# Performance work log

Measured on AMD Instinct MI355X. Metric: run time of the kernel, lower is better.

The kernel has to match this reference:

```python
import jax, jax.numpy as jnp
import numpy as np

HEADS = 16
D_MODEL = 1024
HEAD_DIM = D_MODEL // HEADS


def setup_inputs() -> dict:
    key = jax.random.key(0)
    ks = jax.random.split(key, 11)
    B, S = 4, 2048
    scale_in = 1.0 / np.sqrt(HEAD_DIM)
    scale_out = 1.0 / np.sqrt(D_MODEL)
    return {
        "values": jax.random.normal(ks[0], (B, S, D_MODEL), dtype=jnp.float32),
        "keys": jax.random.normal(ks[1], (B, S, D_MODEL), dtype=jnp.float32),
        "query": jax.random.normal(ks[2], (B, S, D_MODEL), dtype=jnp.float32),
        "wq": jax.random.normal(ks[3], (HEAD_DIM, HEAD_DIM), dtype=jnp.float32) * scale_in,
        "bq": jax.random.normal(ks[4], (HEAD_DIM,), dtype=jnp.float32) * 0.01,
        "wk": jax.random.normal(ks[5], (HEAD_DIM, HEAD_DIM), dtype=jnp.float32) * scale_in,
        "bk": jax.random.normal(ks[6], (HEAD_DIM,), dtype=jnp.float32) * 0.01,
        "wv": jax.random.normal(ks[7], (HEAD_DIM, HEAD_DIM), dtype=jnp.float32) * scale_in,
        "bv": jax.random.normal(ks[8], (HEAD_DIM,), dtype=jnp.float32) * 0.01,
        "wo": jax.random.normal(ks[9], (D_MODEL, D_MODEL), dtype=jnp.float32) * scale_out,
        "bo": jax.random.normal(ks[10], (D_MODEL,), dtype=jnp.float32) * 0.01,
    }


def reference(values, keys, query, wq, bq, wk, bk, wv, bv, wo, bo):
    B, Sq = query.shape[0], query.shape[1]
    Sk, Sv = keys.shape[1], values.shape[1]
    # reshape to (n, s, h, d); per-head linear shares one [d,d] weight across heads
    v = values.reshape(B, Sv, HEADS, HEAD_DIM) @ wv.T + bv
    k = keys.reshape(B, Sk, HEADS, HEAD_DIM) @ wk.T + bk
    q = query.reshape(B, Sq, HEADS, HEAD_DIM) @ wq.T + bq
    # scores scaled by sqrt(d_model) (as in original, NOT sqrt(head_dim))
    energy = jnp.einsum("nqhd,nkhd->nhqk", q, k)
    attn = jax.nn.softmax(energy / jnp.sqrt(jnp.float32(D_MODEL)), axis=-1)
    out = jnp.einsum("nhqk,nkhd->nqhd", attn, v).reshape(B, Sq, D_MODEL)
    return out @ wo.T + bo
```

## Files before the change

### kernel.cpp

```cpp
#include <hip/hip_runtime.h>

typedef unsigned short u16;
typedef short  bfrag  __attribute__((ext_vector_type(8), may_alias));
typedef unsigned long long ull_a __attribute__((may_alias));
typedef int    int_a  __attribute__((may_alias));
typedef int    i4_a   __attribute__((ext_vector_type(4), may_alias));
typedef float  f4_a   __attribute__((ext_vector_type(4), may_alias));
typedef unsigned u32x2 __attribute__((ext_vector_type(2)));
typedef __attribute__((ext_vector_type(4)))  float facc4;
typedef __attribute__((ext_vector_type(16))) float facc16;

#define SEQ   2048
#define NHEAD 16
#define HD    64
#define DM    1024
#define BH    64
#define NTOK  8192
#define QSC   0.04508422f

#if defined(__has_builtin)
#if __has_builtin(__builtin_amdgcn_cvt_pk_bf16_f32)
#define HAS_CVT_PK 1
#endif
#if __has_builtin(__builtin_amdgcn_permlane32_swap)
#define HAS_PLSWAP 1
#endif
#endif
#ifndef HAS_CVT_PK
#define HAS_CVT_PK 0
#endif
#ifndef HAS_PLSWAP
#define HAS_PLSWAP 0
#endif

__device__ __forceinline__ u16 f2bf(float f){
  union { float f; unsigned u; } x; x.f = f;
  unsigned r = x.u + 0x7FFFu + ((x.u >> 16) & 1u);
  return (u16)(r >> 16);
}
__device__ __forceinline__ unsigned pk2(float a, float b){
#if HAS_CVT_PK
  auto r = __builtin_amdgcn_cvt_pk_bf16_f32(a, b);
  union { decltype(r) v; unsigned u; } x; x.v = r; return x.u;
#else
  return (unsigned)f2bf(a) | ((unsigned)f2bf(b) << 16);
#endif
}
__device__ __forceinline__ unsigned long long pk4(float a, float b, float c, float d){
  return (unsigned long long)pk2(a,b) | ((unsigned long long)pk2(c,d) << 32);
}
__device__ __forceinline__ void swap32(unsigned &a, unsigned &b){
#if HAS_PLSWAP
  u32x2 r = __builtin_amdgcn_permlane32_swap(a, b, false, false);
  a = r[0]; b = r[1];
#else
  int lane = threadIdx.x & 63; int hh = lane >> 5;
  unsigned pa = (unsigned)__shfl_xor((int)a, 32, 64);
  unsigned pb = (unsigned)__shfl_xor((int)b, 32, 64);
  unsigned na = hh ? pb : a;
  unsigned nb = hh ? b  : pa;
  a = na; b = nb;
#endif
}
__device__ __forceinline__ bfrag ld8f(const float* p){
  f4_a a = *(const f4_a*)p;
  f4_a b = *(const f4_a*)(p + 4);
  union { bfrag v; unsigned u[4]; } r;
  r.u[0] = pk2(a[0],a[1]); r.u[1] = pk2(a[2],a[3]);
  r.u[2] = pk2(b[0],b[1]); r.u[3] = pk2(b[2],b[3]);
  return r.v;
}
__device__ __forceinline__ void stage16(const u16* g, u16* l){
  __builtin_amdgcn_global_load_lds((const __attribute__((address_space(1))) void*)g,
                                   (__attribute__((address_space(3))) void*)l, 16, 0, 0);
}

__global__ __launch_bounds__(256) void k_wconv(
  const float* __restrict__ wo, u16* __restrict__ dst)
{
  long i = ((long)blockIdx.x * 256 + threadIdx.x) * 8;
  f4_a a = *(const f4_a*)(wo + i);
  f4_a b = *(const f4_a*)(wo + i + 4);
  ull_a* p = (ull_a*)(dst + i);
  p[0] = pk4(a[0],a[1],a[2],a[3]);
  p[1] = pk4(b[0],b[1],b[2],b[3]);
}

__global__ __launch_bounds__(256, 4) void k_proj(
  const float* __restrict__ vin, const float* __restrict__ kin, const float* __restrict__ qin,
  const float* __restrict__ wq, const float* __restrict__ wk, const float* __restrict__ wv,
  const float* __restrict__ bq, const float* __restrict__ bk, const float* __restrict__ bv,
  u16* __restrict__ qo, u16* __restrict__ ko, u16* __restrict__ vt)
{
  __shared__ __align__(16) u16 LT[128*68];
  int tid = threadIdx.x;
  int wid = tid >> 6, lane = tid & 63;
  int ln = lane & 31, hh = lane >> 5;
  int h  = blockIdx.y;
  int t0 = blockIdx.x * 128;
  int b  = t0 >> 11;
  int s0 = t0 & 2047;
  int bh = b * NHEAD + h;
  int tok = t0 + wid*32 + ln;
  long xoff = (long)tok * DM + h * HD;

  auto run_mm = [&](const float* __restrict__ x, const float* __restrict__ w,
                    facc16* acc){
    bfrag bx[4], aw[2][4];
    #pragma unroll
    for (int ks = 0; ks < 4; ks++)
      bx[ks] = ld8f(x + xoff + ks*16 + hh*8);
    #pragma unroll
    for (int dt = 0; dt < 2; dt++)
      #pragma unroll
      for (int ks = 0; ks < 4; ks++)
        aw[dt][ks] = ld8f(w + (dt*32 + ln)*HD + ks*16 + hh*8);
    #pragma unroll
    for (int dt = 0; dt < 2; dt++){
      facc16 a;
      #pragma unroll
      for (int r = 0; r < 16; r++) a[r] = 0.f;
      #pragma unroll
      for (int ks = 0; ks < 4; ks++)
        a = __builtin_amdgcn_mfma_f32_32x32x16_bf16(aw[dt][ks], bx[ks], a, 0,0,0);
      acc[dt] = a;
    }
  };

  {
    facc16 acc[2]; run_mm(vin, wv, acc);
    int s = s0 + wid*32 + ln;
    long vb = (long)bh * HD * SEQ + s;
    #pragma unroll
    for (int dt = 0; dt < 2; dt++)
      #pragma unroll
      for (int g = 0; g < 4; g++){
        f4_a bb = *(const f4_a*)(bv + dt*32 + g*8 + 4*hh);
        #pragma unroll
        for (int j = 0; j < 4; j++){
          int d = dt*32 + g*8 + 4*hh + j;
          vt[vb + (long)d * SEQ] = f2bf(acc[dt][g*4+j] + bb[j]);
        }
      }
  }

  {
    facc16 acc[2]; run_mm(qin, wq, acc);
    int row = wid*32 + ln;
    #pragma unroll
    for (int dt = 0; dt < 2; dt++)
      #pragma unroll
      for (int g = 0; g < 4; g++){
        f4_a bb = *(const f4_a*)(bq + dt*32 + g*8 + 4*hh);
        *(ull_a*)&LT[row*68 + dt*32 + g*8 + 4*hh] =
          pk4((acc[dt][g*4+0]+bb[0])*QSC, (acc[dt][g*4+1]+bb[1])*QSC,
              (acc[dt][g*4+2]+bb[2])*QSC, (acc[dt][g*4+3]+bb[3])*QSC);
      }
  }
  __syncthreads();
  {
    int rr = tid >> 1, half = tid & 1;
    long gb = ((long)bh * SEQ + s0 + rr) * HD + half*32;
    #pragma unroll
    for (int j = 0; j < 4; j++)
      *(i4_a*)(qo + gb + j*8) = *(const i4_a*)&LT[rr*68 + half*32 + j*8];
  }
  __syncthreads();

  {
    facc16 acc[2]; run_mm(kin, wk, acc);
    int row = wid*32 + ln;
    #pragma unroll
    for (int dt = 0; dt < 2; dt++)
      #pragma unroll
      for (int g = 0; g < 4; g++){
        f4_a bb = *(const f4_a*)(bk + dt*32 + g*8 + 4*hh);
        *(ull_a*)&LT[row*68 + dt*32 + g*8 + 4*hh] =
          pk4(acc[dt][g*4+0]+bb[0], acc[dt][g*4+1]+bb[1],
              acc[dt][g*4+2]+bb[2], acc[dt][g*4+3]+bb[3]);
      }
  }
  __syncthreads();
  {
    int rr = tid >> 1, half = tid & 1;
    long gb = ((long)bh * SEQ + s0 + rr) * HD + half*32;
    #pragma unroll
    for (int j = 0; j < 4; j++)
      *(i4_a*)(ko + gb + j*8) = *(const i4_a*)&LT[rr*68 + half*32 + j*8];
  }
}

__global__ __launch_bounds__(512, 4) void k_attn(
  const u16* __restrict__ qws, const u16* __restrict__ kws, const u16* __restrict__ vt,
  u16* __restrict__ aout)
{
  __shared__ __align__(16) u16 KV[2][2][64*64];
  int tid = threadIdx.x;
  int wid = tid >> 6, lane = tid & 63;
  int ln = lane & 31, hh = lane >> 5;
  int bid = blockIdx.x;
  int xcd = bid & 7, lix = bid >> 3;
  int bh = xcd * 8 + (lix >> 3);
  int q0 = (lix & 7) * 256 + wid * 32;
  long base = (long)bh * SEQ * HD;

  int srow   = lane >> 3;
  int schunk = (lane & 7) ^ srow;

  bfrag qf[4];
  #pragma unroll
  for (int ks = 0; ks < 4; ks++)
    qf[ks] = *(const bfrag*)(qws + base + (long)(q0 + ln)*HD + ks*16 + hh*8);

  facc16 OO0, OO1;
  #pragma unroll
  for (int r = 0; r < 16; r++){ OO0[r] = 0.f; OO1[r] = 0.f; }
  float l_ = 0.f;

  stage16(kws + base + (long)(wid*8 + srow)*HD + schunk*8,  &KV[0][0][wid*512]);
  stage16(vt  + base + (long)(wid*8 + srow)*SEQ + schunk*8, &KV[0][1][wid*512]);

  auto tile = [&](int buf, int kt){
    __syncthreads();
    if (kt + 1 < 32){
      int k0n = (kt + 1) * 64;
      stage16(kws + base + (long)(k0n + wid*8 + srow)*HD + schunk*8, &KV[buf^1][0][wid*512]);
      stage16(vt  + base + (long)(wid*8 + srow)*SEQ + k0n + schunk*8, &KV[buf^1][1][wid*512]);
    }

    facc16 E0, E1;
    #pragma unroll
    for (int r = 0; r < 16; r++){ E0[r] = 0.f; E1[r] = 0.f; }
    __builtin_amdgcn_s_setprio(1);
    #pragma unroll
    for (int ks = 0; ks < 4; ks++){
      int sw = ((2*ks + hh) ^ (ln & 7)) * 8;
      bfrag kf0 = *(const bfrag*)&KV[buf][0][ ln      *64 + sw];
      bfrag kf1 = *(const bfrag*)&KV[buf][0][(32 + ln)*64 + sw];
      E0 = __builtin_amdgcn_mfma_f32_32x32x16_bf16(kf0, qf[ks], E0, 0,0,0);
      E1 = __builtin_amdgcn_mfma_f32_32x32x16_bf16(kf1, qf[ks], E1, 0,0,0);
    }
    __builtin_amdgcn_s_setprio(0);

    float rs = 0.f;
    #pragma unroll
    for (int r = 0; r < 16; r++){
      float p0 = __builtin_amdgcn_exp2f(E0[r]);
      float p1 = __builtin_amdgcn_exp2f(E1[r]);
      E0[r] = p0; E1[r] = p1; rs += p0 + p1;
    }
    l_ += rs;

    bfrag pf[4];
    #pragma unroll
    for (int half = 0; half < 2; half++){
      const facc16& P = half ? E1 : E0;
      #pragma unroll
      for (int k2 = 0; k2 < 2; k2++){
        int rb = k2 * 8;
        unsigned A0 = pk2(P[rb+0], P[rb+1]);
        unsigned A1 = pk2(P[rb+2], P[rb+3]);
        unsigned B0 = pk2(P[rb+4], P[rb+5]);
        unsigned B1 = pk2(P[rb+6], P[rb+7]);
        swap32(A0, B0);
        swap32(A1, B1);
        union { bfrag v; unsigned u[4]; } t;
        t.u[0] = A0; t.u[1] = A1; t.u[2] = B0; t.u[3] = B1;
        pf[half*2 + k2] = t.v;
      }
    }

    __builtin_amdgcn_s_setprio(1);
    #pragma unroll
    for (int ks = 0; ks < 4; ks++){
      int sw = ((2*ks + hh) ^ (ln & 7)) * 8;
      bfrag vf0 = *(const bfrag*)&KV[buf][1][ ln      *64 + sw];
      bfrag vf1 = *(const bfrag*)&KV[buf][1][(32 + ln)*64 + sw];
      OO0 = __builtin_amdgcn_mfma_f32_32x32x16_bf16(vf0, pf[ks], OO0, 0,0,0);
      OO1 = __builtin_amdgcn_mfma_f32_32x32x16_bf16(vf1, pf[ks], OO1, 0,0,0);
    }
    __builtin_amdgcn_s_setprio(0);
  };

  for (int kt = 0; kt < 32; kt += 2){
    tile(0, kt);
    tile(1, kt + 1);
  }

  l_ += __shfl_xor(l_, 32, 64);
  float inv = 1.0f / l_;
  int b_ = bh >> 4, h_ = bh & 15;
  long orow = ((long)(b_ * SEQ + q0 + ln) * NHEAD + h_) * HD;
  #pragma unroll
  for (int g = 0; g < 4; g++){
    *(ull_a*)(aout + orow +      8*g + 4*hh) =
      pk4(OO0[4*g]*inv, OO0[4*g+1]*inv, OO0[4*g+2]*inv, OO0[4*g+3]*inv);
    *(ull_a*)(aout + orow + 32 + 8*g + 4*hh) =
      pk4(OO1[4*g]*inv, OO1[4*g+1]*inv, OO1[4*g+2]*inv, OO1[4*g+3]*inv);
  }
}

__global__ __launch_bounds__(256) void k_oproj(
  const u16* __restrict__ A, const u16* __restrict__ Bw,
  const float* __restrict__ bo, float* __restrict__ out)
{
  __shared__ __align__(16) u16 As[128*64];
  __shared__ __align__(16) u16 Bs[128*64];
  int tid  = threadIdx.x;
  int wid  = tid >> 6, lane = tid & 63;
  int quad = lane >> 4, col = lane & 15;
  int m0 = blockIdx.x * 128;
  int n0 = blockIdx.y * 128;
  int wm = (wid & 1) * 64, wn = (wid >> 1) * 64;

  facc4 acc[4][4];
  #pragma unroll
  for (int i = 0; i < 4; i++)
    #pragma unroll
    for (int j = 0; j < 4; j++) acc[i][j] = {0.f,0.f,0.f,0.f};

  int srow = wid*8 + (lane >> 3);
  int scol = (lane & 7) * 8;
  const u16* Ag = A  + (long)(m0 + srow) * DM + scol;
  const u16* Bg = Bw + (long)(n0 + srow) * DM + scol;

  for (int k0 = 0; k0 < DM; k0 += 64){
    __syncthreads();
    #pragma unroll
    for (int j = 0; j < 4; j++){
      stage16(Ag + (long)j*32*DM + k0, &As[(j*32 + wid*8)*64]);
      stage16(Bg + (long)j*32*DM + k0, &Bs[(j*32 + wid*8)*64]);
    }
    __syncthreads();

    #pragma unroll
    for (int ks = 0; ks < 2; ks++){
      bfrag af[4], bf[4];
      #pragma unroll
      for (int i = 0; i < 4; i++)
        af[i] = *(const bfrag*)&As[(wm + i*16 + col)*64 + ks*32 + quad*8];
      #pragma unroll
      for (int i = 0; i < 4; i++)
        bf[i] = *(const bfrag*)&Bs[(wn + i*16 + col)*64 + ks*32 + quad*8];
      #pragma unroll
      for (int i = 0; i < 4; i++)
        #pragma unroll
        for (int j = 0; j < 4; j++)
          acc[i][j] = __builtin_amdgcn_mfma_f32_16x16x32_bf16(af[i], bf[j], acc[i][j], 0,0,0);
    }
  }

  #pragma unroll
  for (int j = 0; j < 4; j++){
    int n = n0 + wn + j*16 + col;
    float bias = bo[n];
    #pragma unroll
    for (int i = 0; i < 4; i++){
      long mrow = m0 + wm + i*16 + quad*4;
      #pragma unroll
      for (int r = 0; r < 4; r++)
        out[(mrow + r) * DM + n] = acc[i][j][r] + bias;
    }
  }
}

extern "C" void kernel_launch(void* const* d_in, const int* in_sizes, int n_in,
                              void* d_out, int out_size, void* d_ws, size_t ws_size,
                              hipStream_t stream)
{
  const float* values = (const float*)d_in[0];
  const float* keys   = (const float*)d_in[1];
  const float* query  = (const float*)d_in[2];
  const float* wq = (const float*)d_in[3];
  const float* bq = (const float*)d_in[4];
  const float* wk = (const float*)d_in[5];
  const float* bk = (const float*)d_in[6];
  const float* wv = (const float*)d_in[7];
  const float* bv = (const float*)d_in[8];
  const float* wo = (const float*)d_in[9];
  const float* bo = (const float*)d_in[10];

  const long N = 8388608;
  u16* qws  = (u16*)d_ws;
  u16* kws  = qws  + N;
  u16* vws  = kws  + N;
  u16* vtws = vws  + N;
  u16* wob  = vtws + N;
  u16* aws  = vws;

  k_wconv <<<512,           256, 0, stream>>>(wo, wob);
  k_proj  <<<dim3(64, 16),  256, 0, stream>>>(values, keys, query, wq, wk, wv,
                                              bq, bk, bv, qws, kws, vtws);
  k_attn  <<<512,           512, 0, stream>>>(qws, kws, vtws, aws);
  k_oproj <<<dim3(64, 8),   256, 0, stream>>>(aws, wob, bo, (float*)d_out);
}
```

Before: 288.3 us.

## Double-buffer LDS, swizzle shared layout, and XCD-aware tile mapping in output projection

Turns the output-projection GEMM's shared-memory staging into a two-buffer pipeline, so the next K-tile's global loads are issued before the current tile's MFMAs and one barrier per step is removed. It also XOR-swizzles the 16-byte chunks in LDS to reduce bank conflicts on fragment reads. Block indices are remapped so each XCD handles a contiguous band of M rows for better L2 reuse. The cost is twice the LDS per block, which may limit occupancy, offset only partly by the launch-bounds hint.

```diff
diff --git a/kernel.cpp b/kernel.cpp
--- a/kernel.cpp
+++ b/kernel.cpp
@@ -300,17 +300,19 @@
   }
 }
 
-__global__ __launch_bounds__(256) void k_oproj(
+__global__ __launch_bounds__(256, 2) void k_oproj(
   const u16* __restrict__ A, const u16* __restrict__ Bw,
   const float* __restrict__ bo, float* __restrict__ out)
 {
-  __shared__ __align__(16) u16 As[128*64];
-  __shared__ __align__(16) u16 Bs[128*64];
+  __shared__ __align__(16) u16 As[2][128*64];
+  __shared__ __align__(16) u16 Bs[2][128*64];
   int tid  = threadIdx.x;
   int wid  = tid >> 6, lane = tid & 63;
   int quad = lane >> 4, col = lane & 15;
-  int m0 = blockIdx.x * 128;
-  int n0 = blockIdx.y * 128;
+  int bid = blockIdx.x;
+  int xcd = bid & 7, lix = bid >> 3;
+  int m0 = (xcd * 8 + (lix >> 3)) * 128;
+  int n0 = (lix & 7) * 128;
   int wm = (wid & 1) * 64, wn = (wid >> 1) * 64;
 
   facc4 acc[4][4];
@@ -319,35 +321,51 @@
     #pragma unroll
     for (int j = 0; j < 4; j++) acc[i][j] = {0.f,0.f,0.f,0.f};
 
-  int srow = wid*8 + (lane >> 3);
-  int scol = (lane & 7) * 8;
-  const u16* Ag = A  + (long)(m0 + srow) * DM + scol;
-  const u16* Bg = Bw + (long)(n0 + srow) * DM + scol;
-
-  for (int k0 = 0; k0 < DM; k0 += 64){
+  int srow   = lane >> 3;
+  int schunk = (lane & 7) ^ srow;
+  const u16* Ag = A  + (long)(m0 + wid*8 + srow) * DM + schunk*8;
+  const u16* Bg = Bw + (long)(n0 + wid*8 + srow) * DM + schunk*8;
+
+  #pragma unroll
+  for (int j = 0; j < 4; j++){
+    stage16(Ag + (long)j*32*DM, &As[0][(j*32 + wid*8)*64]);
+    stage16(Bg + (long)j*32*DM, &Bs[0][(j*32 + wid*8)*64]);
+  }
+
+  auto kstep = [&](int buf, int kt){
     __syncthreads();
-    #pragma unroll
-    for (int j = 0; j < 4; j++){
-      stage16(Ag + (long)j*32*DM + k0, &As[(j*32 + wid*8)*64]);
-      stage16(Bg + (long)j*32*DM + k0, &Bs[(j*32 + wid*8)*64]);
-    }
-    __syncthreads();
-
+    if (kt + 1 < 16){
+      long k0 = (long)(kt + 1) * 64;
+      #pragma unroll
+      for (int j = 0; j < 4; j++){
+        stage16(Ag + (long)j*32*DM + k0, &As[buf^1][(j*32 + wid*8)*64]);
+        stage16(Bg + (long)j*32*DM + k0, &Bs[buf^1][(j*32 + wid*8)*64]);
+      }
+    }
     #pragma unroll
     for (int ks = 0; ks < 2; ks++){
       bfrag af[4], bf[4];
       #pragma unroll
-      for (int i = 0; i < 4; i++)
-        af[i] = *(const bfrag*)&As[(wm + i*16 + col)*64 + ks*32 + quad*8];
-      #pragma unroll
-      for (int i = 0; i < 4; i++)
-        bf[i] = *(const bfrag*)&Bs[(wn + i*16 + col)*64 + ks*32 + quad*8];
+      for (int i = 0; i < 4; i++){
+        int row = wm + i*16 + col;
+        af[i] = *(const bfrag*)&As[buf][row*64 + ((ks*4 + quad) ^ (col & 7))*8];
+      }
+      #pragma unroll
+      for (int i = 0; i < 4; i++){
+        int row = wn + i*16 + col;
+        bf[i] = *(const bfrag*)&Bs[buf][row*64 + ((ks*4 + quad) ^ (col & 7))*8];
+      }
       #pragma unroll
       for (int i = 0; i < 4; i++)
         #pragma unroll
         for (int j = 0; j < 4; j++)
           acc[i][j] = __builtin_amdgcn_mfma_f32_16x16x32_bf16(af[i], bf[j], acc[i][j], 0,0,0);
     }
+  };
+
+  for (int kt = 0; kt < 16; kt += 2){
+    kstep(0, kt);
+    kstep(1, kt + 1);
   }
 
   #pragma unroll
@@ -392,5 +410,5 @@
   k_proj  <<<dim3(64, 16),  256, 0, stream>>>(values, keys, query, wq, wk, wv,
                                               bq, bk, bv, qws, kws, vtws);
   k_attn  <<<512,           512, 0, stream>>>(qws, kws, vtws, aws);
-  k_oproj <<<dim3(64, 8),   256, 0, stream>>>(aws, wob, bo, (float*)d_out);
-}
+  k_oproj <<<512,           256, 0, stream>>>(aws, wob, bo, (float*)d_out);
+}
```

New measurement: 285.2 us. No clear change (-1.1%).
